# Kernel optimization log

Measured on AMD Instinct MI355X. Metric: run time of the kernel, lower is better.

Reference implementation:

```python
import jax, jax.numpy as jnp
import numpy as np

N_HEAD, D_HEAD, D_MODEL = 8, 64, 512
QLEN, MLEN, BSZ = 1024, 1024, 4
KLEN = QLEN + MLEN
SCALE = 1.0 / (D_HEAD ** 0.5)
LN_EPS = 1e-5


def _rel_shift(x):
    # x: [qlen, rlen, bsz, n_head]
    q, rl, b, n = x.shape
    zero_pad = jnp.zeros((q, 1, b, n), x.dtype)
    x_padded = jnp.concatenate([zero_pad, x], axis=1).reshape(rl + 1, q, b, n)
    return x_padded[1:].reshape(q, rl, b, n)


def _layer_norm(x, g, b):
    mu = jnp.mean(x, axis=-1, keepdims=True)
    var = jnp.var(x, axis=-1, keepdims=True)
    return (x - mu) * jax.lax.rsqrt(var + LN_EPS) * g + b


def setup_inputs() -> dict:
    key = jax.random.key(0)
    ks = jax.random.split(key, 10)
    s = 0.02
    return {
        "w": jax.random.normal(ks[0], (QLEN, BSZ, D_MODEL), jnp.float32),
        "r": jax.random.normal(ks[1], (KLEN, 1, D_MODEL), jnp.float32),
        "r_w_bias": jax.random.normal(ks[2], (N_HEAD, D_HEAD), jnp.float32) * s,
        "r_r_bias": jax.random.normal(ks[3], (N_HEAD, D_HEAD), jnp.float32) * s,
        "mems": jax.random.normal(ks[4], (MLEN, BSZ, D_MODEL), jnp.float32),
        "Wq": jax.random.normal(ks[5], (D_MODEL, N_HEAD * D_HEAD), jnp.float32) * s,
        "Wkv": jax.random.normal(ks[6], (D_MODEL, 2 * N_HEAD * D_HEAD), jnp.float32) * s,
        "Wr": jax.random.normal(ks[7], (D_MODEL, N_HEAD * D_HEAD), jnp.float32) * s,
        "Wo": jax.random.normal(ks[8], (N_HEAD * D_HEAD, D_MODEL), jnp.float32) * s,
        "ln_g": jnp.ones((D_MODEL,), jnp.float32),
        "ln_b": jnp.zeros((D_MODEL,), jnp.float32),
        # causal mask: query i can attend keys j <= i + MLEN
        "attn_mask": jnp.arange(KLEN)[None, :] > (jnp.arange(QLEN) + MLEN)[:, None],
    }


def reference(w, r, r_w_bias, r_r_bias, mems, Wq, Wkv, Wr, Wo, ln_g, ln_b, attn_mask):
    qlen, bsz = w.shape[0], w.shape[1]
    cat = jnp.concatenate([mems, w], axis=0)          # [klen, bsz, d_model]
    klen = cat.shape[0]

    r_head_k = (r[:, 0] @ Wr).reshape(-1, N_HEAD, D_HEAD)   # [rlen, n, d]
    kv = cat @ Wkv                                           # [klen, bsz, 2*n*d]
    w_head_k, w_head_v = jnp.split(kv, 2, axis=-1)
    w_head_q = (cat[-qlen:] @ Wq).reshape(qlen, bsz, N_HEAD, D_HEAD)
    w_head_k = w_head_k.reshape(klen, bsz, N_HEAD, D_HEAD)
    w_head_v = w_head_v.reshape(klen, bsz, N_HEAD, D_HEAD)

    AC = jnp.einsum('ibnd,jbnd->ijbn', w_head_q + r_w_bias, w_head_k)
    BD = jnp.einsum('ibnd,jnd->ijbn', w_head_q + r_r_bias, r_head_k)
    BD = _rel_shift(BD)[:, :klen]

    attn_score = (AC + BD) * SCALE                           # [qlen, klen, bsz, n]
    attn_score = jnp.where(attn_mask[:, :, None, None], -jnp.inf, attn_score)
    attn_prob = jax.nn.softmax(attn_score, axis=1)

    attn_vec = jnp.einsum('ijbn,jbnd->ibnd', attn_prob, w_head_v)
    attn_vec = attn_vec.reshape(qlen, bsz, N_HEAD * D_HEAD)
    attn_out = attn_vec @ Wo
    return _layer_norm(w + attn_out, ln_g, ln_b)
```

## Files before the change

kernel.cpp:

```cpp
#include <hip/hip_runtime.h>
#include <hip/hip_bf16.h>
#include <math.h>

#define QLEN 1024
#define MLEN 1024
#define KLEN 2048
#define BSZ 4
#define NH 8
#define DH 64
#define DM 512
#define SCALE 0.125f
#define LN_EPS 1e-5f

#define RK_ROWS 2112

typedef __attribute__((ext_vector_type(8))) short short8;
typedef __attribute__((ext_vector_type(4))) float float4_;

#define GLB(p) ((const __attribute__((address_space(1))) void*)(p))
#define LDSP(p) ((__attribute__((address_space(3))) void*)(p))

__device__ inline ushort to_bf16(float x) {
  __hip_bfloat16 h = __float2bfloat16(x);
  return *reinterpret_cast<ushort*>(&h);
}

__device__ inline float row_max16(float v) {
  int x = __builtin_bit_cast(int, v);
  v = fmaxf(v, __builtin_bit_cast(float, __builtin_amdgcn_update_dpp(x, x, 0xB1, 0xF, 0xF, false)));
  x = __builtin_bit_cast(int, v);
  v = fmaxf(v, __builtin_bit_cast(float, __builtin_amdgcn_update_dpp(x, x, 0x4E, 0xF, 0xF, false)));
  x = __builtin_bit_cast(int, v);
  v = fmaxf(v, __builtin_bit_cast(float, __builtin_amdgcn_update_dpp(x, x, 0x124, 0xF, 0xF, false)));
  x = __builtin_bit_cast(int, v);
  v = fmaxf(v, __builtin_bit_cast(float, __builtin_amdgcn_update_dpp(x, x, 0x128, 0xF, 0xF, false)));
  return v;
}
__device__ inline float row_sum16(float v) {
  int x = __builtin_bit_cast(int, v);
  v += __builtin_bit_cast(float, __builtin_amdgcn_update_dpp(x, x, 0xB1, 0xF, 0xF, false));
  x = __builtin_bit_cast(int, v);
  v += __builtin_bit_cast(float, __builtin_amdgcn_update_dpp(x, x, 0x4E, 0xF, 0xF, false));
  x = __builtin_bit_cast(int, v);
  v += __builtin_bit_cast(float, __builtin_amdgcn_update_dpp(x, x, 0x124, 0xF, 0xF, false));
  x = __builtin_bit_cast(int, v);
  v += __builtin_bit_cast(float, __builtin_amdgcn_update_dpp(x, x, 0x128, 0xF, 0xF, false));
  return v;
}

__global__ __launch_bounds__(256) void cvt_bf16(const float* __restrict__ src,
                                                ushort* __restrict__ dst, int n) {
  int i = (blockIdx.x * 256 + threadIdx.x) * 4;
  if (i >= n) return;
  float4 v = *reinterpret_cast<const float4*>(src + i);
  ushort4 o;
  o.x = to_bf16(v.x); o.y = to_bf16(v.y); o.z = to_bf16(v.z); o.w = to_bf16(v.w);
  *reinterpret_cast<ushort4*>(dst + i) = o;
}

__global__ __launch_bounds__(256) void wtrans(const float* __restrict__ W,
                                              ushort* __restrict__ WT, int N) {
  __shared__ ushort tile[32][33];
  const int k0 = blockIdx.x * 32, n0 = blockIdx.y * 32;
  const int tid = threadIdx.x;
#pragma unroll
  for (int it = 0; it < 4; ++it) {
    int idx = tid + it * 256;
    int r = idx >> 5, c = idx & 31;
    tile[r][c] = to_bf16(W[(size_t)(k0 + r) * N + n0 + c]);
  }
  __syncthreads();
#pragma unroll
  for (int it = 0; it < 4; ++it) {
    int idx = tid + it * 256;
    int r = idx >> 5, c = idx & 31;
    WT[(size_t)(n0 + r) * DM + k0 + c] = tile[c][r];
  }
}

template <int MODE>
__global__ __launch_bounds__(256) void mfma_proj(
    const ushort* __restrict__ A0, const ushort* __restrict__ A1,
    const ushort* __restrict__ BT,
    const float* __restrict__ bias0, const float* __restrict__ bias1,
    ushort* __restrict__ O0, ushort* __restrict__ O1) {
  __shared__ ushort As[128 * 32];
  __shared__ ushort Bs[128 * 32];
  const int tid = threadIdx.x;
  const int m0 = blockIdx.x * 128, n0 = blockIdx.y * 128;
  const int wv = tid >> 6, lane = tid & 63;
  const int wm = wv >> 1, wn = wv & 1;
  const int l16 = lane & 15, quad = lane >> 4;

  const int arow = tid >> 1;
  const int acol = (tid & 1) * 16;
  const ushort* asrc;
  {
    int m = m0 + arow;
    if (MODE == 1)
      asrc = (m < QLEN * BSZ) ? A0 + (size_t)m * DM : A1 + (size_t)(m - QLEN * BSZ) * DM;
    else
      asrc = A0 + (size_t)m * DM;
    asrc += acol;
  }
  const ushort* bsrc = BT + (size_t)(n0 + arow) * DM + acol;

  float4_ acc[4][4];
#pragma unroll
  for (int a = 0; a < 4; ++a)
#pragma unroll
    for (int b = 0; b < 4; ++b) acc[a][b] = float4_{0.f, 0.f, 0.f, 0.f};

  for (int k0 = 0; k0 < DM; k0 += 32) {
    *reinterpret_cast<uint4*>(&As[arow * 32 + acol]) =
        *reinterpret_cast<const uint4*>(asrc + k0);
    *reinterpret_cast<uint4*>(&As[arow * 32 + acol + 8]) =
        *reinterpret_cast<const uint4*>(asrc + k0 + 8);
    *reinterpret_cast<uint4*>(&Bs[arow * 32 + acol]) =
        *reinterpret_cast<const uint4*>(bsrc + k0);
    *reinterpret_cast<uint4*>(&Bs[arow * 32 + acol + 8]) =
        *reinterpret_cast<const uint4*>(bsrc + k0 + 8);
    __syncthreads();
    short8 af[4], bf[4];
#pragma unroll
    for (int f = 0; f < 4; ++f) {
      af[f] = *reinterpret_cast<const short8*>(&As[(wm * 64 + f * 16 + l16) * 32 + quad * 8]);
      bf[f] = *reinterpret_cast<const short8*>(&Bs[(wn * 64 + f * 16 + l16) * 32 + quad * 8]);
    }
#pragma unroll
    for (int fm = 0; fm < 4; ++fm)
#pragma unroll
      for (int fn = 0; fn < 4; ++fn)
        acc[fm][fn] = __builtin_amdgcn_mfma_f32_16x16x32_bf16(af[fm], bf[fn], acc[fm][fn], 0, 0, 0);
    __syncthreads();
  }

#pragma unroll
  for (int fm = 0; fm < 4; ++fm) {
#pragma unroll
    for (int fn = 0; fn < 4; ++fn) {
#pragma unroll
      for (int reg = 0; reg < 4; ++reg) {
        int mm = m0 + wm * 64 + fm * 16 + quad * 4 + reg;
        int nn = n0 + wn * 64 + fn * 16 + l16;
        float v = acc[fm][fn][reg];
        if (MODE == 0) {
          int i = mm >> 2, b = mm & 3;
          int n = nn >> 6, d = nn & 63;
          size_t idx = (((size_t)(b * NH + n)) * QLEN + i) * DH + d;
          O0[idx] = to_bf16(v + bias0[nn]);
          O1[idx] = to_bf16(v + bias1[nn]);
        } else if (MODE == 1) {
          int pos = mm >> 2, b = mm & 3;
          int nn2 = nn & 511;
          int n = nn2 >> 6, d = nn2 & 63;
          size_t idx = (((size_t)(b * NH + n)) * KLEN + pos) * DH + d;
          if (nn < DM) O0[idx] = to_bf16(v);
          else         O1[idx] = to_bf16(v);
        } else {
          int n = nn >> 6, d = nn & 63;
          int cb = d >> 3;
          int dcol = ((cb ^ (mm & 7)) << 3) | (d & 7);
          O0[((size_t)n * RK_ROWS + mm) * DH + dcol] = to_bf16(v);
        }
      }
    }
  }
}

__global__ __launch_bounds__(256) void attn_pack(
    const ushort* __restrict__ kh, const ushort* __restrict__ vrow,
    ushort* __restrict__ k2, ushort* __restrict__ v2) {
  const int jb = blockIdx.x;
  const int bn = blockIdx.y;
  const int tid = threadIdx.x;
  const int i = tid >> 6;
  const int l = tid & 63;
  if (blockIdx.z == 0) {
    int h = i >> 1, c = i & 1;
    const ushort* src = kh + ((size_t)bn * KLEN + jb * 32 + h * 16 + (l & 15)) * DH +
                        c * 32 + (l >> 4) * 8;
    ushort* dst = k2 + ((((size_t)bn * 64 + jb) * 4 + i) * 64 + l) * 8;
    *reinterpret_cast<uint4*>(dst) = *reinterpret_cast<const uint4*>(src);
  } else {
    ushort tmp[8];
    const ushort* srcb = vrow + ((size_t)bn * KLEN + jb * 32 + (l >> 4) * 8) * DH +
                         i * 16 + (l & 15);
#pragma unroll
    for (int u = 0; u < 8; ++u) tmp[u] = srcb[(size_t)u * DH];
    ushort* dst = v2 + ((((size_t)bn * 64 + jb) * 4 + i) * 64 + l) * 8;
    *reinterpret_cast<uint4*>(dst) = *reinterpret_cast<uint4*>(tmp);
  }
}

__global__ __launch_bounds__(256) void mfma_out(
    const ushort* __restrict__ A, const ushort* __restrict__ BT,
    float* __restrict__ Y) {
  __shared__ ushort As[128 * 32];
  __shared__ ushort Bs[128 * 32];
  const int tid = threadIdx.x;
  const int m0 = blockIdx.x * 128, n0 = blockIdx.y * 128;
  const int wv = tid >> 6, lane = tid & 63;
  const int wm = wv >> 1, wn = wv & 1;
  const int l16 = lane & 15, quad = lane >> 4;
  const int arow = tid >> 1;
  const int acol = (tid & 1) * 16;
  const ushort* asrc = A + (size_t)(m0 + arow) * DM + acol;
  const ushort* bsrc = BT + (size_t)(n0 + arow) * DM + acol;

  float4_ acc[4][4];
#pragma unroll
  for (int a = 0; a < 4; ++a)
#pragma unroll
    for (int b = 0; b < 4; ++b) acc[a][b] = float4_{0.f, 0.f, 0.f, 0.f};

  for (int k0 = 0; k0 < DM; k0 += 32) {
    *reinterpret_cast<uint4*>(&As[arow * 32 + acol]) = *reinterpret_cast<const uint4*>(asrc + k0);
    *reinterpret_cast<uint4*>(&As[arow * 32 + acol + 8]) = *reinterpret_cast<const uint4*>(asrc + k0 + 8);
    *reinterpret_cast<uint4*>(&Bs[arow * 32 + acol]) = *reinterpret_cast<const uint4*>(bsrc + k0);
    *reinterpret_cast<uint4*>(&Bs[arow * 32 + acol + 8]) = *reinterpret_cast<const uint4*>(bsrc + k0 + 8);
    __syncthreads();
    short8 af[4], bf[4];
#pragma unroll
    for (int f = 0; f < 4; ++f) {
      af[f] = *reinterpret_cast<const short8*>(&As[(wm * 64 + f * 16 + l16) * 32 + quad * 8]);
      bf[f] = *reinterpret_cast<const short8*>(&Bs[(wn * 64 + f * 16 + l16) * 32 + quad * 8]);
    }
#pragma unroll
    for (int fm = 0; fm < 4; ++fm)
#pragma unroll
      for (int fn = 0; fn < 4; ++fn)
        acc[fm][fn] = __builtin_amdgcn_mfma_f32_16x16x32_bf16(af[fm], bf[fn], acc[fm][fn], 0, 0, 0);
    __syncthreads();
  }
#pragma unroll
  for (int fm = 0; fm < 4; ++fm)
#pragma unroll
    for (int fn = 0; fn < 4; ++fn)
#pragma unroll
      for (int reg = 0; reg < 4; ++reg) {
        int mm = m0 + wm * 64 + fm * 16 + quad * 4 + reg;
        int nn = n0 + wn * 64 + fn * 16 + l16;
        Y[(size_t)mm * DM + nn] = acc[fm][fn][reg];
      }
}

__global__ __launch_bounds__(256) void ln_fuse(
    const float* __restrict__ y, const float* __restrict__ wres,
    const float* __restrict__ g, const float* __restrict__ bb,
    float* __restrict__ out) {
  const int row = blockIdx.x * 4 + (threadIdx.x >> 6);
  const int lane = threadIdx.x & 63;
  const float* yr = y + (size_t)row * DM + lane * 4;
  const float* wr = wres + (size_t)row * DM + lane * 4;
  float4 x0 = *(const float4*)yr;
  float4 x1 = *(const float4*)(yr + 256);
  float4 w0 = *(const float4*)wr;
  float4 w1 = *(const float4*)(wr + 256);
  x0.x += w0.x; x0.y += w0.y; x0.z += w0.z; x0.w += w0.w;
  x1.x += w1.x; x1.y += w1.y; x1.z += w1.z; x1.w += w1.w;
  float s = x0.x + x0.y + x0.z + x0.w + x1.x + x1.y + x1.z + x1.w;
  float ss = x0.x * x0.x + x0.y * x0.y + x0.z * x0.z + x0.w * x0.w +
             x1.x * x1.x + x1.y * x1.y + x1.z * x1.z + x1.w * x1.w;
#pragma unroll
  for (int off = 1; off <= 32; off <<= 1) {
    s += __shfl_xor(s, off, 64);
    ss += __shfl_xor(ss, off, 64);
  }
  float mu = s * (1.f / DM);
  float var = ss * (1.f / DM) - mu * mu;
  float rstd = rsqrtf(var + LN_EPS);
  float4 g0 = *(const float4*)(g + lane * 4);
  float4 g1 = *(const float4*)(g + lane * 4 + 256);
  float4 b0 = *(const float4*)(bb + lane * 4);
  float4 b1 = *(const float4*)(bb + lane * 4 + 256);
  float4 o0, o1;
  o0.x = (x0.x - mu) * rstd * g0.x + b0.x;
  o0.y = (x0.y - mu) * rstd * g0.y + b0.y;
  o0.z = (x0.z - mu) * rstd * g0.z + b0.z;
  o0.w = (x0.w - mu) * rstd * g0.w + b0.w;
  o1.x = (x1.x - mu) * rstd * g1.x + b1.x;
  o1.y = (x1.y - mu) * rstd * g1.y + b1.y;
  o1.z = (x1.z - mu) * rstd * g1.z + b1.z;
  o1.w = (x1.w - mu) * rstd * g1.w + b1.w;
  float* orow = out + (size_t)row * DM + lane * 4;
  *reinterpret_cast<float4*>(orow) = o0;
  *reinterpret_cast<float4*>(orow + 256) = o1;
}

__global__ __launch_bounds__(256) void attn_mfma(
    const ushort* __restrict__ qw, const ushort* __restrict__ qr,
    const ushort* __restrict__ k2, const ushort* __restrict__ v2,
    const ushort* __restrict__ rk2, ushort* __restrict__ avbf) {
  const int i0b = (gridDim.x - 1 - blockIdx.x) * 64;
  const int n = blockIdx.y, b = blockIdx.z;
  const int bn = b * NH + n;
  const int tid = threadIdx.x;
  const int wv = tid >> 6, lane = tid & 63;
  const int l16 = lane & 15, quad = lane >> 4;
  const int i0w = i0b + wv * 16;

  __shared__ ushort stage[2][20 * 512];
  __shared__ float Dlds[4][16 * 66];
  __shared__ ushort Plds[4][16 * 32];
  float* __restrict__ Dw = Dlds[wv];
  ushort* __restrict__ Pw = Plds[wv];

  const ushort* __restrict__ k2b = k2 + (size_t)bn * (64 * 4 * 512);
  const ushort* __restrict__ v2b = v2 + (size_t)bn * (64 * 4 * 512);
  const ushort* __restrict__ rk2n = rk2 + (size_t)n * RK_ROWS * DH;

  const int nIter = (i0b + 63 + MLEN) / 32 + 1;

  short8 aqw0, aqw1, aqr0, aqr1;
  {
    const ushort* qwp = qw + (((size_t)bn * QLEN) + i0w + l16) * DH + quad * 8;
    const ushort* qrp = qr + (((size_t)bn * QLEN) + i0w + l16) * DH + quad * 8;
    aqw0 = *(const short8*)(qwp);
    aqw1 = *(const short8*)(qwp + 32);
    aqr0 = *(const short8*)(qrp);
    aqr1 = *(const short8*)(qrp + 32);
  }

  auto issue_dma = [&](int jb, int buf) {
    const int tbase = jb * 32 - i0b + 960;
#pragma unroll
    for (int s = 0; s < 5; ++s) {
      const int m = wv + s * 4;
      const ushort* g;
      if (m < 8) {
        const ushort* base = (m < 4) ? k2b : v2b;
        g = base + ((size_t)jb * 4 + (m & 3)) * 512 + lane * 8;
      } else {
        int tr = tbase + (m - 8) * 8 + (lane >> 3);
        g = rk2n + (size_t)tr * DH + (lane & 7) * 8;
      }
      __builtin_amdgcn_global_load_lds(GLB(g), LDSP(&stage[buf][m * 512]), 16, 0, 0);
    }
  };

  float4_ O[4];
#pragma unroll
  for (int t = 0; t < 4; ++t) O[t] = float4_{0.f, 0.f, 0.f, 0.f};
  float mrow[4] = {-INFINITY, -INFINITY, -INFINITY, -INFINITY};
  float lpart[4] = {0.f, 0.f, 0.f, 0.f};
  const float SL2E = SCALE * 1.44269504088896f;
  const int rbase = 48 - 16 * wv;
  const int sw = (l16 & 7);

  issue_dma(0, 0);
  issue_dma(1 < nIter ? 1 : 0, 1);

  for (int k = 0; k < nIter; ++k) {
    __builtin_amdgcn_s_waitcnt(0x0F75);
    __builtin_amdgcn_sched_barrier(0);
    __builtin_amdgcn_s_barrier();
    __builtin_amdgcn_sched_barrier(0);
    const ushort* sb = stage[k & 1];
    const int j0 = k * 32;

    float4_ ac[2];
#pragma unroll
    for (int h = 0; h < 2; ++h) {
      short8 b0 = *(const short8*)(sb + (h * 2 + 0) * 512 + lane * 8);
      short8 b1 = *(const short8*)(sb + (h * 2 + 1) * 512 + lane * 8);
      float4_ c = {0.f, 0.f, 0.f, 0.f};
      c = __builtin_amdgcn_mfma_f32_16x16x32_bf16(aqw0, b0, c, 0, 0, 0);
      c = __builtin_amdgcn_mfma_f32_16x16x32_bf16(aqw1, b1, c, 0, 0, 0);
      ac[h] = c;
    }
#pragma unroll
    for (int tt = 0; tt < 3; ++tt) {
      int rowLoc = rbase + tt * 16 + l16;
      const ushort* rrow = sb + 4096 + rowLoc * 64;
      short8 b0 = *(const short8*)(rrow + (((0 + quad) ^ sw) << 3));
      short8 b1 = *(const short8*)(rrow + (((4 + quad) ^ sw) << 3));
      float4_ d = {0.f, 0.f, 0.f, 0.f};
      d = __builtin_amdgcn_mfma_f32_16x16x32_bf16(aqr0, b0, d, 0, 0, 0);
      d = __builtin_amdgcn_mfma_f32_16x16x32_bf16(aqr1, b1, d, 0, 0, 0);
#pragma unroll
      for (int rg = 0; rg < 4; ++rg) {
        int row = quad * 4 + rg;
        Dw[row * 66 + tt * 16 + l16 + row] = d[rg];
      }
    }
    float s[2][4];
#pragma unroll
    for (int half = 0; half < 2; ++half) {
#pragma unroll
      for (int rg = 0; rg < 4; ++rg) {
        int row = quad * 4 + rg;
        int jloc = half * 16 + l16;
        float bd = Dw[row * 66 + jloc + 15];
        float sv = (ac[half][rg] + bd) * SL2E;
        s[half][rg] = (j0 + jloc > i0w + row + MLEN) ? -INFINITY : sv;
      }
    }
#pragma unroll
    for (int rg = 0; rg < 4; ++rg) {
      float mx = row_max16(fmaxf(s[0][rg], s[1][rg]));
      float mn = fmaxf(mrow[rg], mx);
      float alpha = __builtin_amdgcn_exp2f(mrow[rg] - mn);
      float p0 = __builtin_amdgcn_exp2f(s[0][rg] - mn);
      float p1 = __builtin_amdgcn_exp2f(s[1][rg] - mn);
      lpart[rg] = lpart[rg] * alpha + (p0 + p1);
      mrow[rg] = mn;
#pragma unroll
      for (int t = 0; t < 4; ++t) O[t][rg] *= alpha;
      int row = quad * 4 + rg;
      int idx0 = (l16 >> 3) * 128 + row * 8 + (l16 & 7);
      Pw[idx0] = to_bf16(p0);
      Pw[idx0 + 256] = to_bf16(p1);
    }
    short8 pfrag = *(const short8*)(Pw + lane * 8);
#pragma unroll
    for (int t = 0; t < 4; ++t) {
      short8 vfrag = *(const short8*)(sb + (4 + t) * 512 + lane * 8);
      O[t] = __builtin_amdgcn_mfma_f32_16x16x32_bf16(pfrag, vfrag, O[t], 0, 0, 0);
    }

    __builtin_amdgcn_sched_barrier(0);
    __builtin_amdgcn_s_barrier();
    __builtin_amdgcn_sched_barrier(0);
    int jn = k + 2;
    if (jn > nIter - 1) jn = nIter - 1;
    issue_dma(jn, k & 1);
  }

  float inv[4];
#pragma unroll
  for (int rg = 0; rg < 4; ++rg) inv[rg] = 1.f / row_sum16(lpart[rg]);
#pragma unroll
  for (int t = 0; t < 4; ++t)
#pragma unroll
    for (int rg = 0; rg < 4; ++rg) {
      int row = quad * 4 + rg;
      avbf[((size_t)(i0w + row) * BSZ + b) * DM + n * DH + t * 16 + l16] =
          to_bf16(O[t][rg] * inv[rg]);
    }
}

extern "C" void kernel_launch(void* const* d_in, const int* in_sizes, int n_in,
                              void* d_out, int out_size, void* d_ws, size_t ws_size,
                              hipStream_t stream) {
  const float* w    = (const float*)d_in[0];
  const float* r    = (const float*)d_in[1];
  const float* rwb  = (const float*)d_in[2];
  const float* rrb  = (const float*)d_in[3];
  const float* mems = (const float*)d_in[4];
  const float* Wq   = (const float*)d_in[5];
  const float* Wkv  = (const float*)d_in[6];
  const float* Wr   = (const float*)d_in[7];
  const float* Wo   = (const float*)d_in[8];
  const float* ln_g = (const float*)d_in[9];
  const float* ln_b = (const float*)d_in[10];
  float* out = (float*)d_out;

  char* p = (char*)d_ws;
  auto alloc = [&](size_t bytes) {
    char* q = p;
    p += (bytes + 255) & ~(size_t)255;
    return q;
  };
  ushort* wbf   = (ushort*)alloc((size_t)QLEN * BSZ * DM * 2);
  ushort* membf = (ushort*)alloc((size_t)MLEN * BSZ * DM * 2);
  ushort* rbf   = (ushort*)alloc((size_t)KLEN * DM * 2);
  ushort* WqT   = (ushort*)alloc((size_t)DM * DM * 2);
  ushort* WkvT  = (ushort*)alloc((size_t)2 * DM * DM * 2);
  ushort* WrT   = (ushort*)alloc((size_t)DM * DM * 2);
  ushort* WoT   = (ushort*)alloc((size_t)DM * DM * 2);
  ushort* qw    = (ushort*)alloc((size_t)BSZ * NH * QLEN * DH * 2);
  ushort* qr    = (ushort*)alloc((size_t)BSZ * NH * QLEN * DH * 2);
  ushort* kh    = (ushort*)alloc((size_t)BSZ * NH * KLEN * DH * 2);
  ushort* vrow  = (ushort*)alloc((size_t)BSZ * NH * KLEN * DH * 2);
  ushort* k2    = (ushort*)alloc((size_t)BSZ * NH * 64 * 4 * 512 * 2);
  ushort* v2    = (ushort*)alloc((size_t)BSZ * NH * 64 * 4 * 512 * 2);
  ushort* rk2   = (ushort*)alloc((size_t)NH * RK_ROWS * DH * 2);
  float*  y    = (float*)kh;
  ushort* avbf = wbf;

  cvt_bf16<<<dim3(QLEN * BSZ * DM / 1024), dim3(256), 0, stream>>>(w, wbf, QLEN * BSZ * DM);
  cvt_bf16<<<dim3(MLEN * BSZ * DM / 1024), dim3(256), 0, stream>>>(mems, membf, MLEN * BSZ * DM);
  cvt_bf16<<<dim3(KLEN * DM / 1024), dim3(256), 0, stream>>>(r, rbf, KLEN * DM);
  wtrans<<<dim3(16, 16), dim3(256), 0, stream>>>(Wq, WqT, DM);
  wtrans<<<dim3(16, 32), dim3(256), 0, stream>>>(Wkv, WkvT, 2 * DM);
  wtrans<<<dim3(16, 16), dim3(256), 0, stream>>>(Wr, WrT, DM);
  wtrans<<<dim3(16, 16), dim3(256), 0, stream>>>(Wo, WoT, DM);

  mfma_proj<0><<<dim3(32, 4), dim3(256), 0, stream>>>(wbf, nullptr, WqT, rwb, rrb, qw, qr);
  mfma_proj<1><<<dim3(64, 8), dim3(256), 0, stream>>>(membf, wbf, WkvT, nullptr, nullptr, kh, vrow);
  mfma_proj<2><<<dim3(16, 4), dim3(256), 0, stream>>>(rbf, nullptr, WrT, nullptr, nullptr, rk2, nullptr);
  attn_pack<<<dim3(64, 32, 2), dim3(256), 0, stream>>>(kh, vrow, k2, v2);

  attn_mfma<<<dim3(QLEN / 64, NH, BSZ), dim3(256), 0, stream>>>(qw, qr, k2, v2, rk2, avbf);

  mfma_out<<<dim3(32, 4), dim3(256), 0, stream>>>(avbf, WoT, y);
  ln_fuse<<<dim3(QLEN * BSZ / 4), dim3(256), 0, stream>>>(y, w, ln_g, ln_b, out);
}
```

Before: 272.2 us.

## Fuse prep launches and write K/V directly in packed attention layout

The three float-to-bf16 conversion launches are merged into one kernel, and the four weight-transpose launches into one 3D-grid kernel. The KV projection epilogue now scatters K and V straight into the tiled k2/v2 layouts the attention kernel reads, so the separate attn_pack pass and its intermediate kh/vrow buffers go away. This cuts kernel launches and one round trip of K/V through memory, at the cost of scattered 2-byte stores in the projection epilogue. The output buffer y now aliases k2 instead of kh.

```diff
diff --git a/kernel.cpp b/kernel.cpp
--- a/kernel.cpp
+++ b/kernel.cpp
@@ -48,20 +48,45 @@
   return v;
 }
 
-__global__ __launch_bounds__(256) void cvt_bf16(const float* __restrict__ src,
-                                                ushort* __restrict__ dst, int n) {
-  int i = (blockIdx.x * 256 + threadIdx.x) * 4;
-  if (i >= n) return;
-  float4 v = *reinterpret_cast<const float4*>(src + i);
+#define W_ELEMS   (QLEN * BSZ * DM)
+#define MEM_ELEMS (MLEN * BSZ * DM)
+#define R_ELEMS   (KLEN * DM)
+__global__ __launch_bounds__(256) void prep_cvt(
+    const float* __restrict__ w, const float* __restrict__ mems,
+    const float* __restrict__ r, ushort* __restrict__ wbf,
+    ushort* __restrict__ membf, ushort* __restrict__ rbf) {
+  size_t i = ((size_t)blockIdx.x * 256 + threadIdx.x) * 4;
+  const float* src;
+  ushort* dst;
+  if (i < W_ELEMS) {
+    src = w + i; dst = wbf + i;
+  } else if (i < W_ELEMS + MEM_ELEMS) {
+    src = mems + (i - W_ELEMS); dst = membf + (i - W_ELEMS);
+  } else {
+    src = r + (i - W_ELEMS - MEM_ELEMS); dst = rbf + (i - W_ELEMS - MEM_ELEMS);
+  }
+  float4 v = *reinterpret_cast<const float4*>(src);
   ushort4 o;
   o.x = to_bf16(v.x); o.y = to_bf16(v.y); o.z = to_bf16(v.z); o.w = to_bf16(v.w);
-  *reinterpret_cast<ushort4*>(dst + i) = o;
-}
-
-__global__ __launch_bounds__(256) void wtrans(const float* __restrict__ W,
-                                              ushort* __restrict__ WT, int N) {
+  *reinterpret_cast<ushort4*>(dst) = o;
+}
+
+__global__ __launch_bounds__(256) void wtrans_all(
+    const float* __restrict__ Wq, const float* __restrict__ Wkv,
+    const float* __restrict__ Wr, const float* __restrict__ Wo,
+    ushort* __restrict__ WqT, ushort* __restrict__ WkvT,
+    ushort* __restrict__ WrT, ushort* __restrict__ WoT) {
   __shared__ ushort tile[32][33];
+  const int z = blockIdx.z;
+  const float* W;
+  ushort* WT;
+  int N;
+  if (z == 0)      { W = Wq;  WT = WqT;  N = DM; }
+  else if (z == 1) { W = Wkv; WT = WkvT; N = 2 * DM; }
+  else if (z == 2) { W = Wr;  WT = WrT;  N = DM; }
+  else             { W = Wo;  WT = WoT;  N = DM; }
   const int k0 = blockIdx.x * 32, n0 = blockIdx.y * 32;
+  if (n0 >= N) return;
   const int tid = threadIdx.x;
 #pragma unroll
   for (int it = 0; it < 4; ++it) {
@@ -154,9 +179,19 @@
           int pos = mm >> 2, b = mm & 3;
           int nn2 = nn & 511;
           int n = nn2 >> 6, d = nn2 & 63;
-          size_t idx = (((size_t)(b * NH + n)) * KLEN + pos) * DH + d;
-          if (nn < DM) O0[idx] = to_bf16(v);
-          else         O1[idx] = to_bf16(v);
+          int bn = b * NH + n;
+          int jb = pos >> 5, jj = pos & 31;
+          if (nn < DM) {
+            int tile = ((jj >> 4) << 1) | (d >> 5);
+            int lane2 = (((d >> 3) & 3) << 4) | (jj & 15);
+            O0[((((size_t)bn * 64 + jb) * 4 + tile) * 64 + lane2) * 8 + (d & 7)] =
+                to_bf16(v);
+          } else {
+            int tile = d >> 4;
+            int lane2 = ((jj >> 3) << 4) | (d & 15);
+            O1[((((size_t)bn * 64 + jb) * 4 + tile) * 64 + lane2) * 8 + (jj & 7)] =
+                to_bf16(v);
+          }
         } else {
           int n = nn >> 6, d = nn & 63;
           int cb = d >> 3;
@@ -165,31 +200,6 @@
         }
       }
     }
-  }
-}
-
-__global__ __launch_bounds__(256) void attn_pack(
-    const ushort* __restrict__ kh, const ushort* __restrict__ vrow,
-    ushort* __restrict__ k2, ushort* __restrict__ v2) {
-  const int jb = blockIdx.x;
-  const int bn = blockIdx.y;
-  const int tid = threadIdx.x;
-  const int i = tid >> 6;
-  const int l = tid & 63;
-  if (blockIdx.z == 0) {
-    int h = i >> 1, c = i & 1;
-    const ushort* src = kh + ((size_t)bn * KLEN + jb * 32 + h * 16 + (l & 15)) * DH +
-                        c * 32 + (l >> 4) * 8;
-    ushort* dst = k2 + ((((size_t)bn * 64 + jb) * 4 + i) * 64 + l) * 8;
-    *reinterpret_cast<uint4*>(dst) = *reinterpret_cast<const uint4*>(src);
-  } else {
-    ushort tmp[8];
-    const ushort* srcb = vrow + ((size_t)bn * KLEN + jb * 32 + (l >> 4) * 8) * DH +
-                         i * 16 + (l & 15);
-#pragma unroll
-    for (int u = 0; u < 8; ++u) tmp[u] = srcb[(size_t)u * DH];
-    ushort* dst = v2 + ((((size_t)bn * 64 + jb) * 4 + i) * 64 + l) * 8;
-    *reinterpret_cast<uint4*>(dst) = *reinterpret_cast<uint4*>(tmp);
   }
 }
 
@@ -462,35 +472,29 @@
     p += (bytes + 255) & ~(size_t)255;
     return q;
   };
-  ushort* wbf   = (ushort*)alloc((size_t)QLEN * BSZ * DM * 2);
-  ushort* membf = (ushort*)alloc((size_t)MLEN * BSZ * DM * 2);
-  ushort* rbf   = (ushort*)alloc((size_t)KLEN * DM * 2);
+  ushort* wbf   = (ushort*)alloc((size_t)W_ELEMS * 2);
+  ushort* membf = (ushort*)alloc((size_t)MEM_ELEMS * 2);
+  ushort* rbf   = (ushort*)alloc((size_t)R_ELEMS * 2);
   ushort* WqT   = (ushort*)alloc((size_t)DM * DM * 2);
   ushort* WkvT  = (ushort*)alloc((size_t)2 * DM * DM * 2);
   ushort* WrT   = (ushort*)alloc((size_t)DM * DM * 2);
   ushort* WoT   = (ushort*)alloc((size_t)DM * DM * 2);
   ushort* qw    = (ushort*)alloc((size_t)BSZ * NH * QLEN * DH * 2);
   ushort* qr    = (ushort*)alloc((size_t)BSZ * NH * QLEN * DH * 2);
-  ushort* kh    = (ushort*)alloc((size_t)BSZ * NH * KLEN * DH * 2);
-  ushort* vrow  = (ushort*)alloc((size_t)BSZ * NH * KLEN * DH * 2);
   ushort* k2    = (ushort*)alloc((size_t)BSZ * NH * 64 * 4 * 512 * 2);
   ushort* v2    = (ushort*)alloc((size_t)BSZ * NH * 64 * 4 * 512 * 2);
   ushort* rk2   = (ushort*)alloc((size_t)NH * RK_ROWS * DH * 2);
-  float*  y    = (float*)kh;
   ushort* avbf = wbf;
-
-  cvt_bf16<<<dim3(QLEN * BSZ * DM / 1024), dim3(256), 0, stream>>>(w, wbf, QLEN * BSZ * DM);
-  cvt_bf16<<<dim3(MLEN * BSZ * DM / 1024), dim3(256), 0, stream>>>(mems, membf, MLEN * BSZ * DM);
-  cvt_bf16<<<dim3(KLEN * DM / 1024), dim3(256), 0, stream>>>(r, rbf, KLEN * DM);
-  wtrans<<<dim3(16, 16), dim3(256), 0, stream>>>(Wq, WqT, DM);
-  wtrans<<<dim3(16, 32), dim3(256), 0, stream>>>(Wkv, WkvT, 2 * DM);
-  wtrans<<<dim3(16, 16), dim3(256), 0, stream>>>(Wr, WrT, DM);
-  wtrans<<<dim3(16, 16), dim3(256), 0, stream>>>(Wo, WoT, DM);
+  float*  y    = (float*)k2;
+
+  prep_cvt<<<dim3((W_ELEMS + MEM_ELEMS + R_ELEMS) / 1024), dim3(256), 0, stream>>>(
+      w, mems, r, wbf, membf, rbf);
+  wtrans_all<<<dim3(16, 32, 4), dim3(256), 0, stream>>>(
+      Wq, Wkv, Wr, Wo, WqT, WkvT, WrT, WoT);
 
   mfma_proj<0><<<dim3(32, 4), dim3(256), 0, stream>>>(wbf, nullptr, WqT, rwb, rrb, qw, qr);
-  mfma_proj<1><<<dim3(64, 8), dim3(256), 0, stream>>>(membf, wbf, WkvT, nullptr, nullptr, kh, vrow);
+  mfma_proj<1><<<dim3(64, 8), dim3(256), 0, stream>>>(membf, wbf, WkvT, nullptr, nullptr, k2, v2);
   mfma_proj<2><<<dim3(16, 4), dim3(256), 0, stream>>>(rbf, nullptr, WrT, nullptr, nullptr, rk2, nullptr);
-  attn_pack<<<dim3(64, 32, 2), dim3(256), 0, stream>>>(kh, vrow, k2, v2);
 
   attn_mfma<<<dim3(QLEN / 64, NH, BSZ), dim3(256), 0, stream>>>(qw, qr, k2, v2, rk2, avbf);
 
```

After: 262.6 us. -3.5%, faster.
